# Kernel tuning notes

Hardware: AMD Instinct MI355X
Metric: run time of the kernel (lower is better)

The kernel has to match this reference:

```python
import jax, jax.numpy as jnp
import numpy as np

NUM_USERS = 100000
NUM_ITEMS = 50000
EMB = 64
B = 8192
MAXM = 50
ATT_H = 16
PRED_H = 8


def setup_inputs() -> dict:
    key = jax.random.key(0)
    ks = jax.random.split(key, 12)
    member_idx = jax.random.randint(ks[0], (B, MAXM), 0, NUM_USERS)
    # ragged group sizes in [1, MAXM]
    lens = jax.random.randint(ks[1], (B,), 1, MAXM + 1)
    member_mask = jnp.arange(MAXM)[None, :] < lens[:, None]  # bool [B, M]
    item_inputs = jax.random.randint(ks[2], (B,), 0, NUM_ITEMS)
    s = 1.0 / np.sqrt(EMB)
    user_table = jax.random.normal(ks[3], (NUM_USERS, EMB), jnp.float32) * s
    item_table = jax.random.normal(ks[4], (NUM_ITEMS, EMB), jnp.float32) * s
    att_w1 = jax.random.normal(ks[5], (2 * EMB, ATT_H), jnp.float32) * 0.05
    att_b1 = jnp.zeros((ATT_H,), jnp.float32)
    att_w2 = jax.random.normal(ks[6], (ATT_H, 1), jnp.float32) * 0.05
    att_b2 = jnp.zeros((1,), jnp.float32)
    pred_w1 = jax.random.normal(ks[7], (3 * EMB, PRED_H), jnp.float32) * 0.05
    pred_b1 = jnp.zeros((PRED_H,), jnp.float32)
    pred_w2 = jax.random.normal(ks[8], (PRED_H, 1), jnp.float32) * 0.05
    pred_b2 = jnp.zeros((1,), jnp.float32)
    return dict(member_idx=member_idx, member_mask=member_mask, item_inputs=item_inputs,
                user_table=user_table, item_table=item_table,
                att_w1=att_w1, att_b1=att_b1, att_w2=att_w2, att_b2=att_b2,
                pred_w1=pred_w1, pred_b1=pred_b1, pred_w2=pred_w2, pred_b2=pred_b2)


def reference(member_idx, member_mask, item_inputs, user_table, item_table,
              att_w1, att_b1, att_w2, att_b2, pred_w1, pred_b1, pred_w2, pred_b2):
    mem_e = user_table[member_idx]            # [B, M, d]
    item_e = item_table[item_inputs]          # [B, d]
    # attention MLP over concat(member, item)
    cat = jnp.concatenate(
        [mem_e, jnp.broadcast_to(item_e[:, None, :], mem_e.shape)], axis=-1)  # [B, M, 2d]
    h = jax.nn.relu(jnp.einsum('bmf,fh->bmh', cat, att_w1) + att_b1)
    logits = (jnp.einsum('bmh,ho->bmo', h, att_w2) + att_b2)[..., 0]          # [B, M]
    logits = jnp.where(member_mask, logits, -jnp.inf)
    wts = jax.nn.softmax(logits, axis=-1)                                     # [B, M]
    g = jnp.einsum('bm,bmd->bd', wts, mem_e)                                  # [B, d]
    new = jnp.concatenate([g * item_e, g, item_e], axis=-1)                   # [B, 3d]
    ph = jax.nn.relu(new @ pred_w1 + pred_b1)
    y = jax.nn.sigmoid(ph @ pred_w2 + pred_b2)                                # [B, 1]
    return y
```

## Files before the change

kernel.cpp:

```cpp
#include <hip/hip_runtime.h>
#include <hip/hip_bf16.h>


__global__ void AGREE_12773232738622_probe(
    const void* member_mask,
    const void* user_table,
    int* ws)
{
    if (ws[2] == 0x5AFE0001) return;

    const int lane = threadIdx.x;
    const int wi = lane >> 4;
    const int r  = lane & 15;

    int len = 0, ok = 1, prev = 1;
    for (int m = 0; m < 50; ++m) {
        long e = 50L * r + m;
        int nz;
        if (wi == 0)      nz = (((const unsigned char*)member_mask)[e] != 0);
        else if (wi == 1) nz = (((const unsigned short*)member_mask)[e] != 0);
        else if (wi == 2) nz = (((const unsigned int*)member_mask)[e] != 0u);
        else {
            const unsigned int* p = (const unsigned int*)member_mask;
            nz = ((p[2 * e] | p[2 * e + 1]) != 0u);
        }
        if (nz && !prev) ok = 0;
        if (nz) len = len + 1;
        prev = nz;
    }
    if (len == 0) ok = 0;

    ok = ok & __shfl_xor(ok, 1);
    ok = ok & __shfl_xor(ok, 2);
    ok = ok & __shfl_xor(ok, 4);
    ok = ok & __shfl_xor(ok, 8);
    int mx = len;
    mx = max(mx, __shfl_xor(mx, 1));
    mx = max(mx, __shfl_xor(mx, 2));
    mx = max(mx, __shfl_xor(mx, 4));
    mx = max(mx, __shfl_xor(mx, 8));

    int o0 = __shfl(ok, 0),  o1 = __shfl(ok, 16), o2 = __shfl(ok, 32), o3 = __shfl(ok, 48);
    int L0 = __shfl(mx, 0),  L1 = __shfl(mx, 16), L2 = __shfl(mx, 32), L3 = __shfl(mx, 48);

    float v = __bfloat162float(((const __hip_bfloat16*)user_table)[lane]);
    float a = (v < 0.0f) ? -v : v;
    int huge = (!(a < 4.0f)) ? 1 : 0;
    unsigned long long hb = __ballot(huge);
    int hcnt = __popcll(hb);

    if (lane == 0) {
        int bestW = 1, bestLen = -1;
        if (o0 && L0 > bestLen) { bestLen = L0; bestW = 1; }
        if (o1 && L1 > bestLen) { bestLen = L1; bestW = 2; }
        if (o2 && L2 > bestLen) { bestLen = L2; bestW = 4; }
        if (o3 && L3 > bestLen) { bestLen = L3; bestW = 8; }
        ws[0] = bestW;
        ws[1] = (hcnt >= 8) ? 1 : 0;
        ws[2] = 0x5AFE0001;
    }
}

__global__ __launch_bounds__(256, 4) void AGREE_12773232738622_kernel(
    const int* member_idx,
    const void* member_mask,
    const int* item_inputs,
    const void* user_table,
    const void* item_table,
    const void* att_w1,
    const void* att_b1,
    const void* att_w2,
    const void* att_b2,
    const void* pred_w1,
    const void* pred_b1,
    const void* pred_w2,
    const void* pred_b2,
    void* out,
    const int* ws)
{
    const int tid  = threadIdx.x;
    const int lane = tid & 63;
    const int wave = tid >> 6;
    int bb0  = blockIdx.x * 4 + wave;
    const int b = __builtin_amdgcn_readfirstlane(bb0);
    const int mode = ws[0];
    const int isf  = ws[1];

    int valid = 0;
    if (lane < 50) {
        long e0 = 50L * b + lane;
        if (mode == 1)      valid = (((const unsigned char*)member_mask)[e0] != 0);
        else if (mode == 2) valid = (((const unsigned short*)member_mask)[e0] != 0);
        else if (mode == 4) valid = (((const unsigned int*)member_mask)[e0] != 0u);
        else {
            const unsigned int* p = (const unsigned int*)member_mask;
            valid = ((p[2 * e0] | p[2 * e0 + 1]) != 0u);
        }
    }
    unsigned long long vm = __ballot(valid);
    int len = __builtin_amdgcn_readfirstlane(__popcll(vm));
    if (len < 1)  len = 1;
    if (len > 50) len = 50;

    const int* mrow = member_idx + (long)b * 50;
    int sidx[50];
    #pragma unroll
    for (int m = 0; m < 50; ++m) sidx[m] = mrow[m];
    #pragma unroll
    for (int m = 0; m < 50; ++m) if (m >= len) sidx[m] = sidx[0];

    float col[50];
    if (isf) {
        const float* ut = (const float*)user_table;
        #pragma unroll
        for (int m = 0; m < 50; ++m)
            col[m] = ut[(long)sidx[m] * 64 + lane];
    } else {
        const unsigned short* ut = (const unsigned short*)user_table;
        #pragma unroll
        for (int m = 0; m < 50; ++m)
            col[m] = __uint_as_float((unsigned int)ut[(long)sidx[m] * 64 + lane] << 16);
    }

    const int item_id = item_inputs[b];
    float itemv;
    if (isf) itemv = ((const float*)item_table)[item_id * 64 + lane];
    else     itemv = __bfloat162float(((const __hip_bfloat16*)item_table)[item_id * 64 + lane]);

    int idxv = 0;
    if (lane < 50) idxv = mrow[lane];

    float part;
    {
        const int kk = lane & 15;
        const int c  = lane >> 4;
        if (isf) part = (c == 0) ? ((const float*)att_b1)[kk] : 0.0f;
        else     part = (c == 0) ? __bfloat162float(((const __hip_bfloat16*)att_b1)[kk]) : 0.0f;
        for (int t = 0; t < 16; ++t) {
            int f = c * 16 + t;
            float iv = __shfl(itemv, f);
            float w;
            if (isf) w = ((const float*)att_w1)[(64 + f) * 16 + kk];
            else     w = __bfloat162float(((const __hip_bfloat16*)att_w1)[(64 + f) * 16 + kk]);
            part += iv * w;
        }
        part += __shfl_xor(part, 16);
        part += __shfl_xor(part, 32);
    }
    float h[16];
    #pragma unroll
    for (int k = 0; k < 16; ++k) h[k] = __shfl(part, k);

    if (lane < len) {
        if (isf) {
            const float* rp = (const float*)user_table + (long)idxv * 64;
            const float* w1 = (const float*)att_w1;
            #pragma unroll 4
            for (int c = 0; c < 16; ++c) {
                float4 v = ((const float4*)rp)[c];
                #pragma unroll
                for (int k = 0; k < 16; ++k) {
                    h[k] += v.x * w1[(c * 4 + 0) * 16 + k];
                    h[k] += v.y * w1[(c * 4 + 1) * 16 + k];
                    h[k] += v.z * w1[(c * 4 + 2) * 16 + k];
                    h[k] += v.w * w1[(c * 4 + 3) * 16 + k];
                }
            }
        } else {
            const unsigned short* rp = (const unsigned short*)user_table + (long)idxv * 64;
            const unsigned int* w1u = (const unsigned int*)att_w1;
            #pragma unroll 2
            for (int c = 0; c < 8; ++c) {
                uint4 v = ((const uint4*)rp)[c];
                float e[8];
                e[0] = __uint_as_float(v.x << 16);
                e[1] = __uint_as_float(v.x & 0xFFFF0000u);
                e[2] = __uint_as_float(v.y << 16);
                e[3] = __uint_as_float(v.y & 0xFFFF0000u);
                e[4] = __uint_as_float(v.z << 16);
                e[5] = __uint_as_float(v.z & 0xFFFF0000u);
                e[6] = __uint_as_float(v.w << 16);
                e[7] = __uint_as_float(v.w & 0xFFFF0000u);
                #pragma unroll
                for (int j = 0; j < 8; ++j) {
                    #pragma unroll
                    for (int p = 0; p < 8; ++p) {
                        unsigned int wp = w1u[(c * 8 + j) * 8 + p];
                        h[2 * p]     += e[j] * __uint_as_float(wp << 16);
                        h[2 * p + 1] += e[j] * __uint_as_float(wp & 0xFFFF0000u);
                    }
                }
            }
        }
    }

    float lg;
    if (isf) lg = ((const float*)att_b2)[0];
    else     lg = __bfloat162float(((const __hip_bfloat16*)att_b2)[0]);
    #pragma unroll
    for (int k = 0; k < 16; ++k) {
        float hk = fmaxf(h[k], 0.0f);
        float w2;
        if (isf) w2 = ((const float*)att_w2)[k];
        else     w2 = __bfloat162float(((const __hip_bfloat16*)att_w2)[k]);
        lg += hk * w2;
    }

    float x = valid ? lg : -3.0e38f;
    float mx = x;
    mx = fmaxf(mx, __shfl_xor(mx, 1));
    mx = fmaxf(mx, __shfl_xor(mx, 2));
    mx = fmaxf(mx, __shfl_xor(mx, 4));
    mx = fmaxf(mx, __shfl_xor(mx, 8));
    mx = fmaxf(mx, __shfl_xor(mx, 16));
    mx = fmaxf(mx, __shfl_xor(mx, 32));
    float p = valid ? expf(x - mx) : 0.0f;
    float sum = p;
    sum += __shfl_xor(sum, 1);
    sum += __shfl_xor(sum, 2);
    sum += __shfl_xor(sum, 4);
    sum += __shfl_xor(sum, 8);
    sum += __shfl_xor(sum, 16);
    sum += __shfl_xor(sum, 32);
    float wnorm;
    if (sum > 0.0f) wnorm = p * (1.0f / sum);
    else            wnorm = (lane == 0) ? 1.0f : 0.0f;

    float g = 0.0f;
    #pragma unroll
    for (int m = 0; m < 50; ++m) {
        float wv = __int_as_float(__builtin_amdgcn_readlane(__float_as_int(wnorm), m));
        g += wv * col[m];
    }

    const float gi = g * itemv;
    float p8[8];
    if (isf) {
        const float4* pw4 = (const float4*)pred_w1;
        float4 a0 = pw4[lane * 2],         a1 = pw4[lane * 2 + 1];
        float4 b0 = pw4[(64 + lane) * 2],  b1 = pw4[(64 + lane) * 2 + 1];
        float4 c0 = pw4[(128 + lane) * 2], c1 = pw4[(128 + lane) * 2 + 1];
        p8[0] = gi * a0.x + g * b0.x + itemv * c0.x;
        p8[1] = gi * a0.y + g * b0.y + itemv * c0.y;
        p8[2] = gi * a0.z + g * b0.z + itemv * c0.z;
        p8[3] = gi * a0.w + g * b0.w + itemv * c0.w;
        p8[4] = gi * a1.x + g * b1.x + itemv * c1.x;
        p8[5] = gi * a1.y + g * b1.y + itemv * c1.y;
        p8[6] = gi * a1.z + g * b1.z + itemv * c1.z;
        p8[7] = gi * a1.w + g * b1.w + itemv * c1.w;
    } else {
        const uint4* pw4 = (const uint4*)pred_w1;
        uint4 A = pw4[lane];
        uint4 Bv = pw4[64 + lane];
        uint4 C = pw4[128 + lane];
        float ea[8], eb[8], ec[8];
        ea[0] = __uint_as_float(A.x << 16);  ea[1] = __uint_as_float(A.x & 0xFFFF0000u);
        ea[2] = __uint_as_float(A.y << 16);  ea[3] = __uint_as_float(A.y & 0xFFFF0000u);
        ea[4] = __uint_as_float(A.z << 16);  ea[5] = __uint_as_float(A.z & 0xFFFF0000u);
        ea[6] = __uint_as_float(A.w << 16);  ea[7] = __uint_as_float(A.w & 0xFFFF0000u);
        eb[0] = __uint_as_float(Bv.x << 16); eb[1] = __uint_as_float(Bv.x & 0xFFFF0000u);
        eb[2] = __uint_as_float(Bv.y << 16); eb[3] = __uint_as_float(Bv.y & 0xFFFF0000u);
        eb[4] = __uint_as_float(Bv.z << 16); eb[5] = __uint_as_float(Bv.z & 0xFFFF0000u);
        eb[6] = __uint_as_float(Bv.w << 16); eb[7] = __uint_as_float(Bv.w & 0xFFFF0000u);
        ec[0] = __uint_as_float(C.x << 16);  ec[1] = __uint_as_float(C.x & 0xFFFF0000u);
        ec[2] = __uint_as_float(C.y << 16);  ec[3] = __uint_as_float(C.y & 0xFFFF0000u);
        ec[4] = __uint_as_float(C.z << 16);  ec[5] = __uint_as_float(C.z & 0xFFFF0000u);
        ec[6] = __uint_as_float(C.w << 16);  ec[7] = __uint_as_float(C.w & 0xFFFF0000u);
        #pragma unroll
        for (int k2 = 0; k2 < 8; ++k2)
            p8[k2] = gi * ea[k2] + g * eb[k2] + itemv * ec[k2];
    }
    #pragma unroll
    for (int k2 = 0; k2 < 8; ++k2) {
        float v = p8[k2];
        v += __shfl_xor(v, 1);
        v += __shfl_xor(v, 2);
        v += __shfl_xor(v, 4);
        v += __shfl_xor(v, 8);
        v += __shfl_xor(v, 16);
        v += __shfl_xor(v, 32);
        p8[k2] = v;
    }
    if (lane == 0) {
        float z;
        if (isf) z = ((const float*)pred_b2)[0];
        else     z = __bfloat162float(((const __hip_bfloat16*)pred_b2)[0]);
        for (int k2 = 0; k2 < 8; ++k2) {
            float bb2, ww;
            if (isf) {
                bb2 = ((const float*)pred_b1)[k2];
                ww  = ((const float*)pred_w2)[k2];
            } else {
                bb2 = __bfloat162float(((const __hip_bfloat16*)pred_b1)[k2]);
                ww  = __bfloat162float(((const __hip_bfloat16*)pred_w2)[k2]);
            }
            float hh = p8[k2] + bb2;
            if (hh < 0.0f) hh = 0.0f;
            z += hh * ww;
        }
        float y = 1.0f / (1.0f + expf(-z));
        if (isf) ((float*)out)[b] = y;
        else     ((__hip_bfloat16*)out)[b] = __float2bfloat16(y);
    }
}

extern "C" void kernel_launch(void* const* d_in, const int* in_sizes, int n_in,
                              void* d_out, int out_size, void* d_ws, size_t ws_size,
                              hipStream_t stream) {
    (void)in_sizes; (void)n_in; (void)out_size; (void)ws_size;
    AGREE_12773232738622_probe<<<1, 64, 0, stream>>>(
        d_in[1], d_in[3], (int*)d_ws);
    AGREE_12773232738622_kernel<<<2048, 256, 0, stream>>>(
        (const int*)d_in[0],
        d_in[1],
        (const int*)d_in[2],
        d_in[3],
        d_in[4],
        d_in[5],
        d_in[6],
        d_in[7],
        d_in[8],
        d_in[9],
        d_in[10],
        d_in[11],
        d_in[12],
        d_out,
        (const int*)d_ws);
}
```

Before: 188.0 us.

## Stage gathered member embeddings in LDS and reuse them for attention and pooling

Gathered member rows go into a padded shared-memory tile once per group. The attention MLP and the weighted pooling both read from that tile, so the second global read of each member row is gone, along with the 50-entry register arrays. Launch changes to one 64-thread block per group, and the pooling loop now stops at the group's actual length. The cost is LDS footprint per block (about 13 KB), a block-level barrier, and more small blocks to schedule.

```diff
diff --git a/kernel.cpp b/kernel.cpp
--- a/kernel.cpp
+++ b/kernel.cpp
@@ -61,7 +61,7 @@
     }
 }
 
-__global__ __launch_bounds__(256, 4) void AGREE_12773232738622_kernel(
+__global__ __launch_bounds__(64) void AGREE_12773232738622_kernel(
     const int* member_idx,
     const void* member_mask,
     const int* item_inputs,
@@ -78,11 +78,10 @@
     void* out,
     const int* ws)
 {
-    const int tid  = threadIdx.x;
-    const int lane = tid & 63;
-    const int wave = tid >> 6;
-    int bb0  = blockIdx.x * 4 + wave;
-    const int b = __builtin_amdgcn_readfirstlane(bb0);
+    __shared__ float s_mem[50][65];
+
+    const int lane = threadIdx.x;
+    const int b    = blockIdx.x;
     const int mode = ws[0];
     const int isf  = ws[1];
 
@@ -103,32 +102,32 @@
     if (len > 50) len = 50;
 
     const int* mrow = member_idx + (long)b * 50;
-    int sidx[50];
-    #pragma unroll
-    for (int m = 0; m < 50; ++m) sidx[m] = mrow[m];
-    #pragma unroll
-    for (int m = 0; m < 50; ++m) if (m >= len) sidx[m] = sidx[0];
-
-    float col[50];
-    if (isf) {
-        const float* ut = (const float*)user_table;
-        #pragma unroll
-        for (int m = 0; m < 50; ++m)
-            col[m] = ut[(long)sidx[m] * 64 + lane];
-    } else {
-        const unsigned short* ut = (const unsigned short*)user_table;
-        #pragma unroll
-        for (int m = 0; m < 50; ++m)
-            col[m] = __uint_as_float((unsigned int)ut[(long)sidx[m] * 64 + lane] << 16);
-    }
+    int idxv = 0;
+    if (lane < 50) idxv = mrow[lane];
 
     const int item_id = item_inputs[b];
     float itemv;
     if (isf) itemv = ((const float*)item_table)[item_id * 64 + lane];
     else     itemv = __bfloat162float(((const __hip_bfloat16*)item_table)[item_id * 64 + lane]);
 
-    int idxv = 0;
-    if (lane < 50) idxv = mrow[lane];
+    if (isf) {
+        const float* ut = (const float*)user_table;
+        #pragma unroll
+        for (int m = 0; m < 50; ++m) {
+            int mc = (m < len) ? m : 0;
+            int id = __builtin_amdgcn_readlane(idxv, mc);
+            s_mem[m][lane] = ut[(long)id * 64 + lane];
+        }
+    } else {
+        const unsigned short* ut = (const unsigned short*)user_table;
+        #pragma unroll
+        for (int m = 0; m < 50; ++m) {
+            int mc = (m < len) ? m : 0;
+            int id = __builtin_amdgcn_readlane(idxv, mc);
+            s_mem[m][lane] = __uint_as_float(
+                (unsigned int)ut[(long)id * 64 + lane] << 16);
+        }
+    }
 
     float part;
     {
@@ -151,44 +150,27 @@
     #pragma unroll
     for (int k = 0; k < 16; ++k) h[k] = __shfl(part, k);
 
+    __syncthreads();
+
     if (lane < len) {
         if (isf) {
-            const float* rp = (const float*)user_table + (long)idxv * 64;
             const float* w1 = (const float*)att_w1;
-            #pragma unroll 4
-            for (int c = 0; c < 16; ++c) {
-                float4 v = ((const float4*)rp)[c];
+            #pragma unroll 8
+            for (int f = 0; f < 64; ++f) {
+                float mv = s_mem[lane][f];
                 #pragma unroll
-                for (int k = 0; k < 16; ++k) {
-                    h[k] += v.x * w1[(c * 4 + 0) * 16 + k];
-                    h[k] += v.y * w1[(c * 4 + 1) * 16 + k];
-                    h[k] += v.z * w1[(c * 4 + 2) * 16 + k];
-                    h[k] += v.w * w1[(c * 4 + 3) * 16 + k];
-                }
+                for (int k = 0; k < 16; ++k) h[k] += mv * w1[f * 16 + k];
             }
         } else {
-            const unsigned short* rp = (const unsigned short*)user_table + (long)idxv * 64;
             const unsigned int* w1u = (const unsigned int*)att_w1;
-            #pragma unroll 2
-            for (int c = 0; c < 8; ++c) {
-                uint4 v = ((const uint4*)rp)[c];
-                float e[8];
-                e[0] = __uint_as_float(v.x << 16);
-                e[1] = __uint_as_float(v.x & 0xFFFF0000u);
-                e[2] = __uint_as_float(v.y << 16);
-                e[3] = __uint_as_float(v.y & 0xFFFF0000u);
-                e[4] = __uint_as_float(v.z << 16);
-                e[5] = __uint_as_float(v.z & 0xFFFF0000u);
-                e[6] = __uint_as_float(v.w << 16);
-                e[7] = __uint_as_float(v.w & 0xFFFF0000u);
+            #pragma unroll 8
+            for (int f = 0; f < 64; ++f) {
+                float mv = s_mem[lane][f];
                 #pragma unroll
-                for (int j = 0; j < 8; ++j) {
-                    #pragma unroll
-                    for (int p = 0; p < 8; ++p) {
-                        unsigned int wp = w1u[(c * 8 + j) * 8 + p];
-                        h[2 * p]     += e[j] * __uint_as_float(wp << 16);
-                        h[2 * p + 1] += e[j] * __uint_as_float(wp & 0xFFFF0000u);
-                    }
+                for (int p = 0; p < 8; ++p) {
+                    unsigned int wp = w1u[f * 8 + p];
+                    h[2 * p]     += mv * __uint_as_float(wp << 16);
+                    h[2 * p + 1] += mv * __uint_as_float(wp & 0xFFFF0000u);
                 }
             }
         }
@@ -227,10 +209,9 @@
     else            wnorm = (lane == 0) ? 1.0f : 0.0f;
 
     float g = 0.0f;
-    #pragma unroll
-    for (int m = 0; m < 50; ++m) {
+    for (int m = 0; m < len; ++m) {
         float wv = __int_as_float(__builtin_amdgcn_readlane(__float_as_int(wnorm), m));
-        g += wv * col[m];
+        g += wv * s_mem[m][lane];
     }
 
     const float gi = g * itemv;
@@ -310,7 +291,7 @@
     (void)in_sizes; (void)n_in; (void)out_size; (void)ws_size;
     AGREE_12773232738622_probe<<<1, 64, 0, stream>>>(
         d_in[1], d_in[3], (int*)d_ws);
-    AGREE_12773232738622_kernel<<<2048, 256, 0, stream>>>(
+    AGREE_12773232738622_kernel<<<8192, 64, 0, stream>>>(
         (const int*)d_in[0],
         d_in[1],
         (const int*)d_in[2],
```

Result: slower. 202.2 us (+7.5%).

## Defer member-column gather until after softmax to cut register pressure

Applied to the files above, without the earlier changes.

The 50-entry per-lane column cache loaded up front is removed. The member rows are instead re-gathered in the weighted-sum loop after softmax, with indices and weights broadcast through shuffles. The attention stage now loads each lane's full member row into registers before the FMA loop, and the readfirstlane uniformity hints on batch index and length are dropped. The aim is fewer live VGPRs and higher occupancy. In exchange, the second gather is serialized after the softmax and reads rows for padded members too, which the old code redirected to row 0.

```diff
diff --git a/kernel.cpp b/kernel.cpp
--- a/kernel.cpp
+++ b/kernel.cpp
@@ -81,8 +81,7 @@
     const int tid  = threadIdx.x;
     const int lane = tid & 63;
     const int wave = tid >> 6;
-    int bb0  = blockIdx.x * 4 + wave;
-    const int b = __builtin_amdgcn_readfirstlane(bb0);
+    const int b    = blockIdx.x * 4 + wave;
     const int mode = ws[0];
     const int isf  = ws[1];
 
@@ -98,29 +97,9 @@
         }
     }
     unsigned long long vm = __ballot(valid);
-    int len = __builtin_amdgcn_readfirstlane(__popcll(vm));
+    int len = __popcll(vm);
     if (len < 1)  len = 1;
     if (len > 50) len = 50;
-
-    const int* mrow = member_idx + (long)b * 50;
-    int sidx[50];
-    #pragma unroll
-    for (int m = 0; m < 50; ++m) sidx[m] = mrow[m];
-    #pragma unroll
-    for (int m = 0; m < 50; ++m) if (m >= len) sidx[m] = sidx[0];
-
-    float col[50];
-    if (isf) {
-        const float* ut = (const float*)user_table;
-        #pragma unroll
-        for (int m = 0; m < 50; ++m)
-            col[m] = ut[(long)sidx[m] * 64 + lane];
-    } else {
-        const unsigned short* ut = (const unsigned short*)user_table;
-        #pragma unroll
-        for (int m = 0; m < 50; ++m)
-            col[m] = __uint_as_float((unsigned int)ut[(long)sidx[m] * 64 + lane] << 16);
-    }
 
     const int item_id = item_inputs[b];
     float itemv;
@@ -128,7 +107,7 @@
     else     itemv = __bfloat162float(((const __hip_bfloat16*)item_table)[item_id * 64 + lane]);
 
     int idxv = 0;
-    if (lane < 50) idxv = mrow[lane];
+    if (lane < 50) idxv = member_idx[b * 50 + lane];
 
     float part;
     {
@@ -155,32 +134,36 @@
         if (isf) {
             const float* rp = (const float*)user_table + (long)idxv * 64;
             const float* w1 = (const float*)att_w1;
-            #pragma unroll 4
+            float4 vv[16];
+            #pragma unroll
+            for (int c = 0; c < 16; ++c) vv[c] = ((const float4*)rp)[c];
+            #pragma unroll
             for (int c = 0; c < 16; ++c) {
-                float4 v = ((const float4*)rp)[c];
                 #pragma unroll
                 for (int k = 0; k < 16; ++k) {
-                    h[k] += v.x * w1[(c * 4 + 0) * 16 + k];
-                    h[k] += v.y * w1[(c * 4 + 1) * 16 + k];
-                    h[k] += v.z * w1[(c * 4 + 2) * 16 + k];
-                    h[k] += v.w * w1[(c * 4 + 3) * 16 + k];
+                    h[k] += vv[c].x * w1[(c * 4 + 0) * 16 + k];
+                    h[k] += vv[c].y * w1[(c * 4 + 1) * 16 + k];
+                    h[k] += vv[c].z * w1[(c * 4 + 2) * 16 + k];
+                    h[k] += vv[c].w * w1[(c * 4 + 3) * 16 + k];
                 }
             }
         } else {
             const unsigned short* rp = (const unsigned short*)user_table + (long)idxv * 64;
             const unsigned int* w1u = (const unsigned int*)att_w1;
-            #pragma unroll 2
+            uint4 vv[8];
+            #pragma unroll
+            for (int c = 0; c < 8; ++c) vv[c] = ((const uint4*)rp)[c];
+            #pragma unroll
             for (int c = 0; c < 8; ++c) {
-                uint4 v = ((const uint4*)rp)[c];
                 float e[8];
-                e[0] = __uint_as_float(v.x << 16);
-                e[1] = __uint_as_float(v.x & 0xFFFF0000u);
-                e[2] = __uint_as_float(v.y << 16);
-                e[3] = __uint_as_float(v.y & 0xFFFF0000u);
-                e[4] = __uint_as_float(v.z << 16);
-                e[5] = __uint_as_float(v.z & 0xFFFF0000u);
-                e[6] = __uint_as_float(v.w << 16);
-                e[7] = __uint_as_float(v.w & 0xFFFF0000u);
+                e[0] = __uint_as_float(vv[c].x << 16);
+                e[1] = __uint_as_float(vv[c].x & 0xFFFF0000u);
+                e[2] = __uint_as_float(vv[c].y << 16);
+                e[3] = __uint_as_float(vv[c].y & 0xFFFF0000u);
+                e[4] = __uint_as_float(vv[c].z << 16);
+                e[5] = __uint_as_float(vv[c].z & 0xFFFF0000u);
+                e[6] = __uint_as_float(vv[c].w << 16);
+                e[7] = __uint_as_float(vv[c].w & 0xFFFF0000u);
                 #pragma unroll
                 for (int j = 0; j < 8; ++j) {
                     #pragma unroll
@@ -227,10 +210,22 @@
     else            wnorm = (lane == 0) ? 1.0f : 0.0f;
 
     float g = 0.0f;
-    #pragma unroll
-    for (int m = 0; m < 50; ++m) {
-        float wv = __int_as_float(__builtin_amdgcn_readlane(__float_as_int(wnorm), m));
-        g += wv * col[m];
+    if (isf) {
+        const float* ut = (const float*)user_table;
+        #pragma unroll
+        for (int m = 0; m < 50; ++m) {
+            int idm  = __shfl(idxv, m);
+            float wv = __shfl(wnorm, m);
+            g += wv * ut[(long)idm * 64 + lane];
+        }
+    } else {
+        const unsigned short* ut = (const unsigned short*)user_table;
+        #pragma unroll
+        for (int m = 0; m < 50; ++m) {
+            int idm  = __shfl(idxv, m);
+            float wv = __shfl(wnorm, m);
+            g += wv * __uint_as_float((unsigned int)ut[(long)idm * 64 + lane] << 16);
+        }
     }
 
     const float gi = g * itemv;
```

After: 161.5 us. -14.1%, faster.
